# Kernel tuning notes

Measured on AMD Instinct MI355X. Metric: run time of the kernel, lower is better.

Reference implementation:

```python
import jax, jax.numpy as jnp
import numpy as np

D_MODEL = 1024
NUM_HEADS = 16
D_K = D_MODEL // NUM_HEADS
ROPE_THETA = 10000.0
BATCH = 4
SEQ = 2048


def _trunc_normal(key, shape):
    # approx of torch.nn.init.trunc_normal_ (std=1, truncated to [-2, 2])
    return jnp.clip(jax.random.truncated_normal(key, -2.0, 2.0, shape, jnp.float32), -2.0, 2.0)


def setup_inputs() -> dict:
    key = jax.random.key(0)
    kx, kq, kk, kv, ko = jax.random.split(key, 5)
    x = jax.random.normal(kx, (BATCH, SEQ, D_MODEL), jnp.float32)
    token_positions = jnp.broadcast_to(jnp.arange(SEQ, dtype=jnp.int32), (BATCH, SEQ))
    return {
        "x": x,
        "token_positions": token_positions,
        "q_proj": _trunc_normal(kq, (D_MODEL, D_MODEL)),
        "k_proj": _trunc_normal(kk, (D_MODEL, D_MODEL)),
        "v_proj": _trunc_normal(kv, (D_MODEL, D_MODEL)),
        "o_proj": _trunc_normal(ko, (D_MODEL, D_MODEL)),
    }


def _rope(t, positions):
    # t: [b, h, s, k], positions: [b, s]
    half = D_K // 2
    inv_freq = 1.0 / (ROPE_THETA ** (jnp.arange(half, dtype=jnp.float32) * 2.0 / D_K))
    ang = positions.astype(jnp.float32)[:, None, :, None] * inv_freq  # [b,1,s,half]
    cos, sin = jnp.cos(ang), jnp.sin(ang)
    t1 = t[..., 0::2]
    t2 = t[..., 1::2]
    r1 = t1 * cos - t2 * sin
    r2 = t1 * sin + t2 * cos
    return jnp.stack([r1, r2], axis=-1).reshape(t.shape)


def reference(x, token_positions, q_proj, k_proj, v_proj, o_proj):
    b, s, d = x.shape
    Wq = q_proj.reshape(NUM_HEADS, D_K, d)
    Wk = k_proj.reshape(NUM_HEADS, D_K, d)
    Wv = v_proj.reshape(NUM_HEADS, D_K, d)
    Wo = o_proj.reshape(d, NUM_HEADS, D_K).transpose(1, 0, 2)  # h d k
    Q = jnp.einsum('bsd,hkd->bhsk', x, Wq)
    K = jnp.einsum('bsd,hkd->bhsk', x, Wk)
    V = jnp.einsum('bsd,hkd->bhsk', x, Wv)
    Q = _rope(Q, token_positions)
    K = _rope(K, token_positions)
    scale = 1.0 / jnp.sqrt(jnp.asarray(D_K, jnp.float32))
    scores = jnp.einsum('bhqk,bhsk->bhqs', Q, K) * scale  # [b,h,s,s]
    causal = jnp.tril(jnp.ones((s, s), dtype=bool))
    scores = jnp.where(causal, scores, -jnp.inf)
    attn = jax.nn.softmax(scores, axis=-1)
    O = jnp.einsum('bhqs,bhsk->bhqk', attn, V)
    return jnp.einsum('bhsk,hdk->bsd', O, Wo)
```

## Files before the change

kernel.cpp:

```cpp
#include <hip/hip_runtime.h>
#include <cmath>


typedef __bf16 bf16_t;
typedef __bf16 bf16x2 __attribute__((ext_vector_type(2)));
typedef __bf16 bf16x4 __attribute__((ext_vector_type(4)));
typedef __bf16 bf16x8 __attribute__((ext_vector_type(8)));
typedef float f32x2 __attribute__((ext_vector_type(2)));
typedef float f32x4 __attribute__((ext_vector_type(4)));
typedef unsigned int u32;
typedef const __attribute__((address_space(1))) u32* gaddr_t;
typedef __attribute__((address_space(3))) u32* saddr_t;

struct RopeTab { float inv[32]; };

__device__ __forceinline__ void split4(const float* __restrict__ in,
                                       bf16_t* __restrict__ hi,
                                       bf16_t* __restrict__ lo, bool LO,
                                       int blk, int tid)
{
  const int i = blk * 256 + tid;
  const f32x4 u = *(const f32x4*)(in + (size_t)i * 4);
  bf16x4 h, l;
  #pragma unroll
  for (int j = 0; j < 4; ++j) {
    const bf16_t hb = (bf16_t)u[j];
    h[j] = hb;
    if (LO) l[j] = (bf16_t)(u[j] - (float)hb);
  }
  *(bf16x4*)(hi + (size_t)i * 4) = h;
  if (LO) *(bf16x4*)(lo + (size_t)i * 4) = l;
}

__global__ __launch_bounds__(256) void prep_k(
    const float* __restrict__ x,  const float* __restrict__ qw,
    const float* __restrict__ kw, const float* __restrict__ vw,
    const float* __restrict__ ow, RopeTab tab,
    bf16_t* __restrict__ Xh,  bf16_t* __restrict__ Xl,
    bf16_t* __restrict__ QWh, bf16_t* __restrict__ QWl,
    bf16_t* __restrict__ KWh, bf16_t* __restrict__ KWl,
    bf16_t* __restrict__ VWh, bf16_t* __restrict__ OWh,
    float* __restrict__ ropeT)
{
  const int bid = blockIdx.x, tid = threadIdx.x;
  if (bid < 8192)       split4(x,  Xh,  Xl,  true,  bid,         tid);
  else if (bid < 9216)  split4(qw, QWh, QWl, true,  bid - 8192,  tid);
  else if (bid < 10240) split4(kw, KWh, KWl, true,  bid - 9216,  tid);
  else if (bid < 11264) split4(vw, VWh, nullptr, false, bid - 10240, tid);
  else if (bid < 12288) split4(ow, OWh, nullptr, false, bid - 11264, tid);
  else {
    const int i = (bid - 12288) * 256 + tid;
    const int p = i >> 5, d2 = i & 31;
    float sn, cs;
    sincosf((float)p * tab.inv[d2], &sn, &cs);
    ropeT[(size_t)i * 2]     = cs;
    ropeT[(size_t)i * 2 + 1] = sn;
  }
}

__global__ __launch_bounds__(256, 4) void gemm_qkv(
    const bf16_t* __restrict__ Xh, const bf16_t* __restrict__ Xl,
    const bf16_t* __restrict__ QWh, const bf16_t* __restrict__ QWl,
    const bf16_t* __restrict__ KWh, const bf16_t* __restrict__ KWl,
    const bf16_t* __restrict__ VWh,
    const int* __restrict__ tokpos, const float* __restrict__ ropeT,
    bf16_t* __restrict__ Oq_h, bf16_t* __restrict__ Oq_l,
    bf16_t* __restrict__ Ok_h, bf16_t* __restrict__ Ok_l,
    bf16_t* __restrict__ Vt)
{
  __shared__ __align__(16) bf16_t sA[128 * 64];
  __shared__ __align__(16) bf16_t sB[128 * 64];

  const int tid = threadIdx.x;
  const int lane = tid & 63, wv = tid >> 6;
  const int wr = wv >> 1, wc = wv & 1;
  const int la = lane & 15, lb = lane >> 4;
  const int row0 = blockIdx.x * 128, col0 = blockIdx.y * 128;
  const int z = blockIdx.z;

  const int srow = wv * 32 + (lane >> 3);
  const int schk = lane & 7;

  f32x4 acc[4][4] = {};

  const int NT = (z == 2) ? 16 : 48;

  for (int t = 0; t < NT; ++t) {
    const int seg = t >> 4;
    const int k0 = (t & 15) << 6;
    const bf16_t* Ap = (z < 2 && seg == 2) ? Xl : Xh;
    const bf16_t* Wp = (z == 2) ? VWh
                     : (z == 1) ? ((seg == 1) ? KWl : KWh)
                                : ((seg == 1) ? QWl : QWh);
    __syncthreads();
    #pragma unroll
    for (int i = 0; i < 4; ++i) {
      const int r = srow + i * 8;
      const int cs_ = (schk ^ (r & 7)) * 8;
      __builtin_amdgcn_global_load_lds(
          (gaddr_t)(Ap + (size_t)(row0 + r) * 1024 + k0 + cs_),
          (saddr_t)(sA + wv * 2048 + i * 512), 16, 0, 0);
      __builtin_amdgcn_global_load_lds(
          (gaddr_t)(Wp + (size_t)(col0 + r) * 1024 + k0 + cs_),
          (saddr_t)(sB + wv * 2048 + i * 512), 16, 0, 0);
    }
    __syncthreads();

    #pragma unroll
    for (int ks = 0; ks < 2; ++ks) {
      bf16x8 af[4];
      #pragma unroll
      for (int m = 0; m < 4; ++m) {
        const int r = wr * 64 + m * 16 + la;
        af[m] = *(const bf16x8*)&sA[r * 64 + (((ks * 4 + lb) ^ (la & 7)) * 8)];
      }
      #pragma unroll
      for (int n = 0; n < 4; ++n) {
        const int r = wc * 64 + n * 16 + la;
        const bf16x8 bfr = *(const bf16x8*)&sB[r * 64 + (((ks * 4 + lb) ^ (la & 7)) * 8)];
        #pragma unroll
        for (int m = 0; m < 4; ++m)
          acc[m][n] = __builtin_amdgcn_mfma_f32_16x16x32_bf16(af[m], bfr, acc[m][n], 0, 0, 0);
      }
    }
  }

  #pragma unroll
  for (int n = 0; n < 4; ++n) {
    const int gn = col0 + wc * 64 + n * 16 + la;
    #pragma unroll
    for (int m = 0; m < 4; ++m) {
      const int gm0 = row0 + wr * 64 + m * 16 + lb * 4;
      if (z == 2) {
        const int b = gm0 >> 11, s0 = gm0 & 2047;
        const int h = gn >> 6, d = gn & 63;
        bf16x4 v;
        #pragma unroll
        for (int j = 0; j < 4; ++j) v[j] = (bf16_t)acc[m][n][j];
        *(bf16x4*)&Vt[(((size_t)b * 16 + h) * 64 + d) * 2048 + s0] = v;
      } else {
        const int d = gn & 63, h = gn >> 6;
        const bool odd = d & 1;
        bf16_t* Oh = z ? Ok_h : Oq_h;
        bf16_t* Ol = z ? Ok_l : Oq_l;
        #pragma unroll
        for (int j = 0; j < 4; ++j) {
          const int gm = gm0 + j;
          const float t = acc[m][n][j];
          const float other = __shfl_xor(t, 1, 64);
          const int pos = tokpos[gm];
          const f32x2 cs2 = *(const f32x2*)&ropeT[((size_t)pos << 6) + ((d >> 1) << 1)];
          const float r = odd ? (other * cs2[1] + t * cs2[0])
                              : (t * cs2[0] - other * cs2[1]);
          const bf16_t hb = (bf16_t)r;
          const int b = gm >> 11, s = gm & 2047;
          const size_t oi = (((size_t)b * 16 + h) * 2048 + s) * 64 + d;
          Oh[oi] = hb;
          Ol[oi] = (bf16_t)(r - (float)hb);
        }
      }
    }
  }
}

__global__ __launch_bounds__(256, 4) void gemm_o(
    const bf16_t* __restrict__ Ag, const bf16_t* __restrict__ Wg,
    float* __restrict__ Of)
{
  __shared__ __align__(16) bf16_t sA[128 * 64];
  __shared__ __align__(16) bf16_t sB[128 * 64];

  const int tid = threadIdx.x;
  const int lane = tid & 63, wv = tid >> 6;
  const int wr = wv >> 1, wc = wv & 1;
  const int la = lane & 15, lb = lane >> 4;
  const int row0 = blockIdx.x * 128, col0 = blockIdx.y * 128;

  const int srow = wv * 32 + (lane >> 3);
  const int schk = lane & 7;

  f32x4 acc[4][4] = {};

  for (int t = 0; t < 16; ++t) {
    const int k0 = t << 6;
    __syncthreads();
    #pragma unroll
    for (int i = 0; i < 4; ++i) {
      const int r = srow + i * 8;
      const int cs_ = (schk ^ (r & 7)) * 8;
      __builtin_amdgcn_global_load_lds(
          (gaddr_t)(Ag + (size_t)(row0 + r) * 1024 + k0 + cs_),
          (saddr_t)(sA + wv * 2048 + i * 512), 16, 0, 0);
      __builtin_amdgcn_global_load_lds(
          (gaddr_t)(Wg + (size_t)(col0 + r) * 1024 + k0 + cs_),
          (saddr_t)(sB + wv * 2048 + i * 512), 16, 0, 0);
    }
    __syncthreads();
    #pragma unroll
    for (int ks = 0; ks < 2; ++ks) {
      bf16x8 af[4];
      #pragma unroll
      for (int m = 0; m < 4; ++m) {
        const int r = wr * 64 + m * 16 + la;
        af[m] = *(const bf16x8*)&sA[r * 64 + (((ks * 4 + lb) ^ (la & 7)) * 8)];
      }
      #pragma unroll
      for (int n = 0; n < 4; ++n) {
        const int r = wc * 64 + n * 16 + la;
        const bf16x8 bfr = *(const bf16x8*)&sB[r * 64 + (((ks * 4 + lb) ^ (la & 7)) * 8)];
        #pragma unroll
        for (int m = 0; m < 4; ++m)
          acc[m][n] = __builtin_amdgcn_mfma_f32_16x16x32_bf16(af[m], bfr, acc[m][n], 0, 0, 0);
      }
    }
  }

  #pragma unroll
  for (int n = 0; n < 4; ++n) {
    const int gn = col0 + wc * 64 + n * 16 + la;
    #pragma unroll
    for (int m = 0; m < 4; ++m) {
      const int gm0 = row0 + wr * 64 + m * 16 + lb * 4;
      #pragma unroll
      for (int j = 0; j < 4; ++j)
        Of[(size_t)(gm0 + j) * 1024 + gn] = acc[m][n][j];
    }
  }
}

__device__ __forceinline__ int SW(int e) { return e ^ (((e >> 6) & 7) << 3); }

__global__ __launch_bounds__(512, 4) void attn_kernel(
    const bf16_t* __restrict__ Qhi, const bf16_t* __restrict__ Qlo,
    const bf16_t* __restrict__ Khi, const bf16_t* __restrict__ Klo,
    const bf16_t* __restrict__ Vt, bf16_t* __restrict__ O)
{
  __shared__ __align__(16) bf16_t sKV[2][3 * 4096];
  __shared__ __align__(16) bf16_t sP[8 * 1024];

  const int linear = (int)blockIdx.x;
  const int xcd = linear & 7;
  const int pos = linear >> 3;
  const int bh  = xcd * 8 + (pos >> 3);
  const int p   = pos & 7;
  const int b = bh >> 4, h = bh & 15;

  const size_t base = (size_t)bh * 2048 * 64;
  const bf16_t* Qh_ = Qhi + base;
  const bf16_t* Ql_ = Qlo + base;
  const bf16_t* Kh_ = Khi + base;
  const bf16_t* Kl_ = Klo + base;
  const bf16_t* Vt_ = Vt + base;

  const int tid = threadIdx.x, wv = tid >> 6, lane = tid & 63;
  const int la = lane & 15, lb = lane >> 4;

  const int sr   = wv * 8 + (lane >> 3);
  const int scsw = (lane & 7) ^ (sr & 7);
  const int ssrc = sr * 64 + scsw * 8;
  const int se0  = wv * 512;
  const int psw  = (la & 7) << 3;

  auto STAGE = [&](int kvb, int buf) {
    const int kv0 = kvb * 64;
    bf16_t* dst = &sKV[buf][0];
    __builtin_amdgcn_global_load_lds((gaddr_t)(Kh_ + (size_t)kv0 * 64 + ssrc),
                                     (saddr_t)(dst + se0), 16, 0, 0);
    __builtin_amdgcn_global_load_lds((gaddr_t)(Kl_ + (size_t)kv0 * 64 + ssrc),
                                     (saddr_t)(dst + 4096 + se0), 16, 0, 0);
    __builtin_amdgcn_global_load_lds((gaddr_t)(Vt_ + (size_t)sr * 2048 + kv0 + scsw * 8),
                                     (saddr_t)(dst + 8192 + se0), 16, 0, 0);
  };

  for (int half = 0; half < 2; ++half) {
    const int qb = half ? p : 15 - p;
    const int q = qb * 128 + wv * 16 + la;
    bf16x8 qh[2], ql[2];
    #pragma unroll
    for (int kf = 0; kf < 2; ++kf) {
      qh[kf] = *(const bf16x8*)&Qh_[(size_t)q * 64 + kf * 32 + lb * 8];
      ql[kf] = *(const bf16x8*)&Ql_[(size_t)q * 64 + kf * 32 + lb * 8];
    }

    f32x4 oacc[4] = {};
    float m = -1e30f, l = 0.f;
    const int nt = 2 * qb + 2;

    STAGE(0, 0);
    __syncthreads();

    for (int kvb = 0; kvb < nt; ++kvb) {
      const int kv0 = kvb * 64;
      if (kvb + 1 < nt) STAGE(kvb + 1, (kvb + 1) & 1);

      const bf16_t* sKh = &sKV[kvb & 1][0];
      const bf16_t* sKl = sKh + 4096;
      const bf16_t* sVt = sKh + 8192;

      f32x4 sacc[4] = {};
      __builtin_amdgcn_s_setprio(1);
      #pragma unroll
      for (int nf = 0; nf < 4; ++nf) {
        #pragma unroll
        for (int kf = 0; kf < 2; ++kf) {
          const int rr = SW((nf * 16 + la) * 64 + kf * 32 + lb * 8);
          const bf16x8 kh = *(const bf16x8*)&sKh[rr];
          const bf16x8 kl = *(const bf16x8*)&sKl[rr];
          sacc[nf] = __builtin_amdgcn_mfma_f32_16x16x32_bf16(kh, qh[kf], sacc[nf], 0, 0, 0);
          sacc[nf] = __builtin_amdgcn_mfma_f32_16x16x32_bf16(kl, qh[kf], sacc[nf], 0, 0, 0);
          sacc[nf] = __builtin_amdgcn_mfma_f32_16x16x32_bf16(kh, ql[kf], sacc[nf], 0, 0, 0);
        }
      }
      __builtin_amdgcn_s_setprio(0);

      if (kvb >= 2 * qb) {
        #pragma unroll
        for (int nf = 0; nf < 4; ++nf)
          #pragma unroll
          for (int j = 0; j < 4; ++j) {
            const int kvi = kv0 + nf * 16 + lb * 4 + j;
            sacc[nf][j] = (kvi <= q) ? sacc[nf][j] * 0.125f : -1e30f;
          }
      } else {
        #pragma unroll
        for (int nf = 0; nf < 4; ++nf)
          #pragma unroll
          for (int j = 0; j < 4; ++j) sacc[nf][j] *= 0.125f;
      }

      float red = sacc[0][0];
      #pragma unroll
      for (int nf = 0; nf < 4; ++nf)
        #pragma unroll
        for (int j = 0; j < 4; ++j) red = fmaxf(red, sacc[nf][j]);
      red = fmaxf(red, __shfl_xor(red, 16, 64));
      red = fmaxf(red, __shfl_xor(red, 32, 64));

      const float mn = fmaxf(m, red);
      if (!__all(mn - m <= 8.0f)) {
        const float sf = __expf(m - mn);
        m = mn;
        l *= sf;
        #pragma unroll
        for (int nf = 0; nf < 4; ++nf)
          #pragma unroll
          for (int j = 0; j < 4; ++j) oacc[nf][j] *= sf;
      }

      float rs = 0.f;
      #pragma unroll
      for (int nf = 0; nf < 4; ++nf)
        #pragma unroll
        for (int j = 0; j < 4; ++j) {
          const float pj = __expf(sacc[nf][j] - m);
          sacc[nf][j] = pj;
          rs += pj;
        }
      rs += __shfl_xor(rs, 16, 64);
      rs += __shfl_xor(rs, 32, 64);
      l += rs;

      #pragma unroll
      for (int nf = 0; nf < 4; ++nf) {
        bf16x4 pv;
        #pragma unroll
        for (int j = 0; j < 4; ++j) pv[j] = (bf16_t)sacc[nf][j];
        *(bf16x4*)&sP[wv * 1024 + la * 64 + ((nf * 16 + lb * 4) ^ psw)] = pv;
      }

      __builtin_amdgcn_s_setprio(1);
      #pragma unroll
      for (int ks = 0; ks < 2; ++ks) {
        const bf16x8 pa = *(const bf16x8*)&sP[wv * 1024 + la * 64 + ((ks * 32 + lb * 8) ^ psw)];
        #pragma unroll
        for (int nf = 0; nf < 4; ++nf) {
          const bf16x8 vb2 = *(const bf16x8*)&sVt[SW((nf * 16 + la) * 64 + ks * 32 + lb * 8)];
          oacc[nf] = __builtin_amdgcn_mfma_f32_16x16x32_bf16(vb2, pa, oacc[nf], 0, 0, 0);
        }
      }
      __builtin_amdgcn_s_setprio(0);

      __syncthreads();
    }

    const float inv_l = 1.0f / l;
    #pragma unroll
    for (int nf = 0; nf < 4; ++nf) {
      bf16x4 ov;
      #pragma unroll
      for (int j = 0; j < 4; ++j) ov[j] = (bf16_t)(oacc[nf][j] * inv_l);
      const int d0 = nf * 16 + lb * 4;
      *(bf16x4*)&O[(((size_t)b * 2048 + q) * 16 + h) * 64 + d0] = ov;
    }
  }
}

extern "C" void kernel_launch(void* const* d_in, const int* in_sizes, int n_in,
                              void* d_out, int out_size, void* d_ws, size_t ws_size,
                              hipStream_t stream)
{
  const float* x      = (const float*)d_in[0];
  const int*   tokpos = (const int*)d_in[1];
  const float* qw     = (const float*)d_in[2];
  const float* kw     = (const float*)d_in[3];
  const float* vw     = (const float*)d_in[4];
  const float* ow     = (const float*)d_in[5];
  float* out = (float*)d_out;

  const size_t E  = (size_t)4 * 16 * 2048 * 64;
  const size_t W1 = (size_t)1024 * 1024;
  bf16_t* base = (bf16_t*)d_ws;
  bf16_t* Qhi = base;
  bf16_t* Qlo = base + E;
  bf16_t* Khi = base + 2 * E;
  bf16_t* Klo = base + 3 * E;
  bf16_t* Vt  = base + 4 * E;
  bf16_t* Xh  = base + 5 * E;
  bf16_t* Xl  = base + 6 * E;
  bf16_t* QWh = base + 7 * E;
  bf16_t* QWl = QWh + W1;
  bf16_t* KWh = QWh + 2 * W1;
  bf16_t* KWl = QWh + 3 * W1;
  bf16_t* VWh = QWh + 4 * W1;
  bf16_t* OWh = QWh + 5 * W1;
  float*  ropeT = (float*)(QWh + 6 * W1);
  bf16_t* O = Xh;

  RopeTab tab;
  for (int i = 0; i < 32; ++i)
    tab.inv[i] = (float)pow(10000.0, -(double)i / 32.0);

  prep_k<<<12544, 256, 0, stream>>>(x, qw, kw, vw, ow, tab,
                                    Xh, Xl, QWh, QWl, KWh, KWl, VWh, OWh, ropeT);

  gemm_qkv<<<dim3(64, 8, 3), 256, 0, stream>>>(
      Xh, Xl, QWh, QWl, KWh, KWl, VWh, tokpos, ropeT,
      Qhi, Qlo, Khi, Klo, Vt);
  attn_kernel<<<512, 512, 0, stream>>>(Qhi, Qlo, Khi, Klo, Vt, O);
  gemm_o<<<dim3(64, 8), 256, 0, stream>>>(O, OWh, out);
}
```

Measured before the change: 241.7 us.

## Add 256x256 double-buffered Q/K projection GEMM with async LDS loads

The Q and K projections move into a new kernel with 256x256 output tiles, 512 threads, double-buffered shared memory filled by direct global-to-LDS loads, XOR-swizzled layout, tile-index remapping and setprio around the MFMA loop. The V projection stays on the old kernel, launched separately with a z offset. The larger tiles are meant to raise arithmetic intensity and overlap loads with compute. The cost is one block per CU (128 blocks per z slice on a 256-CU part), a second kernel launch, and an epilogue that writes the RoPE'd outputs as scattered scalar stores.

New measurement: 282.0 us. 1.17x slower.

```diff
diff --git a/kernel.cpp b/kernel.cpp
--- a/kernel.cpp
+++ b/kernel.cpp
@@ -58,6 +58,121 @@
   }
 }
 
+__global__ __launch_bounds__(512, 1) void gemm_qk256(
+    const bf16_t* __restrict__ Xh, const bf16_t* __restrict__ Xl,
+    const bf16_t* __restrict__ QWh, const bf16_t* __restrict__ QWl,
+    const bf16_t* __restrict__ KWh, const bf16_t* __restrict__ KWl,
+    const int* __restrict__ tokpos, const float* __restrict__ ropeT,
+    bf16_t* __restrict__ Oq_h, bf16_t* __restrict__ Oq_l,
+    bf16_t* __restrict__ Ok_h, bf16_t* __restrict__ Ok_l)
+{
+  __shared__ __align__(16) bf16_t sA[2][256 * 64];
+  __shared__ __align__(16) bf16_t sB[2][256 * 64];
+
+  const int tid = threadIdx.x;
+  const int lane = tid & 63, wv = tid >> 6;
+  const int wr = wv >> 2, wc = wv & 3;
+  const int la = lane & 15, lb = lane >> 4;
+
+  const int lin  = (int)blockIdx.y * 32 + (int)blockIdx.x;
+  const int lin2 = (lin & 7) * 16 + (lin >> 3);
+  const int bx = lin2 & 31, by = lin2 >> 5;
+  const int row0 = bx * 256, col0 = by * 256;
+  const int z = blockIdx.z;
+
+  const bf16_t* Wh = z ? KWh : QWh;
+  const bf16_t* Wl = z ? KWl : QWl;
+
+  const int sr8  = tid >> 3;
+  const int scsw = (tid & 7) ^ (sr8 & 7);
+
+  f32x4 acc[8][4] = {};
+
+  auto STAGE = [&](int t, int buf) {
+    const int seg = t >> 4;
+    const int k0 = (t & 15) << 6;
+    const bf16_t* Ap = (seg == 2) ? Xl : Xh;
+    const bf16_t* Wp = (seg == 1) ? Wl : Wh;
+    #pragma unroll
+    for (int j = 0; j < 4; ++j) {
+      const int r = j * 64 + sr8;
+      __builtin_amdgcn_global_load_lds(
+          (gaddr_t)(Ap + (size_t)(row0 + r) * 1024 + k0 + scsw * 8),
+          (saddr_t)(&sA[buf][0] + j * 4096 + tid * 8), 16, 0, 0);
+    }
+    #pragma unroll
+    for (int j = 0; j < 4; ++j) {
+      const int r = j * 64 + sr8;
+      __builtin_amdgcn_global_load_lds(
+          (gaddr_t)(Wp + (size_t)(col0 + r) * 1024 + k0 + scsw * 8),
+          (saddr_t)(&sB[buf][0] + j * 4096 + tid * 8), 16, 0, 0);
+    }
+  };
+
+  const int NT = 48;
+  STAGE(0, 0);
+  for (int t = 0; t < NT; ++t) {
+    if (t + 1 < NT) {
+      STAGE(t + 1, (t + 1) & 1);
+      asm volatile("s_waitcnt vmcnt(8)" ::: "memory");
+    } else {
+      asm volatile("s_waitcnt vmcnt(0)" ::: "memory");
+    }
+    __builtin_amdgcn_s_barrier();
+
+    const bf16_t* cA = &sA[t & 1][0];
+    const bf16_t* cB = &sB[t & 1][0];
+    #pragma unroll
+    for (int ks = 0; ks < 2; ++ks) {
+      bf16x8 bfr[4];
+      #pragma unroll
+      for (int nf = 0; nf < 4; ++nf) {
+        const int r = wc * 64 + nf * 16 + la;
+        bfr[nf] = *(const bf16x8*)&cB[r * 64 + (((ks * 4 + lb) ^ (la & 7)) * 8)];
+      }
+      __builtin_amdgcn_s_setprio(1);
+      #pragma unroll
+      for (int mf = 0; mf < 8; ++mf) {
+        const int r = wr * 128 + mf * 16 + la;
+        const bf16x8 a = *(const bf16x8*)&cA[r * 64 + (((ks * 4 + lb) ^ (la & 7)) * 8)];
+        #pragma unroll
+        for (int nf = 0; nf < 4; ++nf)
+          acc[mf][nf] = __builtin_amdgcn_mfma_f32_16x16x32_bf16(a, bfr[nf], acc[mf][nf], 0, 0, 0);
+      }
+      __builtin_amdgcn_s_setprio(0);
+    }
+    __builtin_amdgcn_s_barrier();
+  }
+
+  bf16_t* Oh = z ? Ok_h : Oq_h;
+  bf16_t* Ol = z ? Ok_l : Oq_l;
+  #pragma unroll
+  for (int n = 0; n < 4; ++n) {
+    const int gn = col0 + wc * 64 + n * 16 + la;
+    const int d = gn & 63, h = gn >> 6;
+    const bool odd = d & 1;
+    #pragma unroll
+    for (int m = 0; m < 8; ++m) {
+      const int gm0 = row0 + wr * 128 + m * 16 + lb * 4;
+      #pragma unroll
+      for (int j = 0; j < 4; ++j) {
+        const int gm = gm0 + j;
+        const float t = acc[m][n][j];
+        const float other = __shfl_xor(t, 1, 64);
+        const int pos = tokpos[gm];
+        const f32x2 cs2 = *(const f32x2*)&ropeT[((size_t)pos << 6) + ((d >> 1) << 1)];
+        const float r = odd ? (other * cs2[1] + t * cs2[0])
+                            : (t * cs2[0] - other * cs2[1]);
+        const bf16_t hb = (bf16_t)r;
+        const int b = gm >> 11, s = gm & 2047;
+        const size_t oi = (((size_t)b * 16 + h) * 2048 + s) * 64 + d;
+        Oh[oi] = hb;
+        Ol[oi] = (bf16_t)(r - (float)hb);
+      }
+    }
+  }
+}
+
 __global__ __launch_bounds__(256, 4) void gemm_qkv(
     const bf16_t* __restrict__ Xh, const bf16_t* __restrict__ Xl,
     const bf16_t* __restrict__ QWh, const bf16_t* __restrict__ QWl,
@@ -66,7 +181,7 @@
     const int* __restrict__ tokpos, const float* __restrict__ ropeT,
     bf16_t* __restrict__ Oq_h, bf16_t* __restrict__ Oq_l,
     bf16_t* __restrict__ Ok_h, bf16_t* __restrict__ Ok_l,
-    bf16_t* __restrict__ Vt)
+    bf16_t* __restrict__ Vt, int zbase)
 {
   __shared__ __align__(16) bf16_t sA[128 * 64];
   __shared__ __align__(16) bf16_t sB[128 * 64];
@@ -76,7 +191,7 @@
   const int wr = wv >> 1, wc = wv & 1;
   const int la = lane & 15, lb = lane >> 4;
   const int row0 = blockIdx.x * 128, col0 = blockIdx.y * 128;
-  const int z = blockIdx.z;
+  const int z = blockIdx.z + zbase;
 
   const int srow = wv * 32 + (lane >> 3);
   const int schk = lane & 7;
@@ -433,9 +548,11 @@
   prep_k<<<12544, 256, 0, stream>>>(x, qw, kw, vw, ow, tab,
                                     Xh, Xl, QWh, QWl, KWh, KWl, VWh, OWh, ropeT);
 
-  gemm_qkv<<<dim3(64, 8, 3), 256, 0, stream>>>(
+  gemm_qk256<<<dim3(32, 4, 2), 512, 0, stream>>>(
+      Xh, Xl, QWh, QWl, KWh, KWl, tokpos, ropeT, Qhi, Qlo, Khi, Klo);
+  gemm_qkv<<<dim3(64, 8, 1), 256, 0, stream>>>(
       Xh, Xl, QWh, QWl, KWh, KWl, VWh, tokpos, ropeT,
-      Qhi, Qlo, Khi, Klo, Vt);
+      Qhi, Qlo, Khi, Klo, Vt, 2);
   attn_kernel<<<512, 512, 0, stream>>>(Qhi, Qlo, Khi, Klo, Vt, O);
   gemm_o<<<dim3(64, 8), 256, 0, stream>>>(O, OWh, out);
 }
```

## Fuse Q and K projections into one block sharing the X tile

Applied to the files above, without the earlier changes.

The QKV GEMM now runs with 512-thread blocks. In the z=0 slice, two groups of four waves compute Q and K for the same 128x128 tile and share one staged X tile in LDS, which halves X reloads for the Q/K projections. The V projection uses 8 waves on a 128x128 tile with 4x2 accumulators per wave. The grid shrinks from 3 to 2 z-slices. This costs more LDS per block (48KB) and leaves the two z-slices with unequal work (48 k-steps vs 16), which may hurt load balance.

Result: slower. 249.7 us (+3.3%).

```diff
diff --git a/kernel.cpp b/kernel.cpp
--- a/kernel.cpp
+++ b/kernel.cpp
@@ -58,7 +58,7 @@
   }
 }
 
-__global__ __launch_bounds__(256, 4) void gemm_qkv(
+__global__ __launch_bounds__(512, 4) void gemm_qkv2(
     const bf16_t* __restrict__ Xh, const bf16_t* __restrict__ Xl,
     const bf16_t* __restrict__ QWh, const bf16_t* __restrict__ QWl,
     const bf16_t* __restrict__ KWh, const bf16_t* __restrict__ KWl,
@@ -69,80 +69,75 @@
     bf16_t* __restrict__ Vt)
 {
   __shared__ __align__(16) bf16_t sA[128 * 64];
-  __shared__ __align__(16) bf16_t sB[128 * 64];
+  __shared__ __align__(16) bf16_t sW0[128 * 64];
+  __shared__ __align__(16) bf16_t sW1[128 * 64];
 
   const int tid = threadIdx.x;
   const int lane = tid & 63, wv = tid >> 6;
-  const int wr = wv >> 1, wc = wv & 1;
   const int la = lane & 15, lb = lane >> 4;
   const int row0 = blockIdx.x * 128, col0 = blockIdx.y * 128;
-  const int z = blockIdx.z;
-
-  const int srow = wv * 32 + (lane >> 3);
-  const int schk = lane & 7;
-
-  f32x4 acc[4][4] = {};
-
-  const int NT = (z == 2) ? 16 : 48;
-
-  for (int t = 0; t < NT; ++t) {
-    const int seg = t >> 4;
-    const int k0 = (t & 15) << 6;
-    const bf16_t* Ap = (z < 2 && seg == 2) ? Xl : Xh;
-    const bf16_t* Wp = (z == 2) ? VWh
-                     : (z == 1) ? ((seg == 1) ? KWl : KWh)
-                                : ((seg == 1) ? QWl : QWh);
-    __syncthreads();
-    #pragma unroll
-    for (int i = 0; i < 4; ++i) {
-      const int r = srow + i * 8;
-      const int cs_ = (schk ^ (r & 7)) * 8;
-      __builtin_amdgcn_global_load_lds(
-          (gaddr_t)(Ap + (size_t)(row0 + r) * 1024 + k0 + cs_),
-          (saddr_t)(sA + wv * 2048 + i * 512), 16, 0, 0);
-      __builtin_amdgcn_global_load_lds(
-          (gaddr_t)(Wp + (size_t)(col0 + r) * 1024 + k0 + cs_),
-          (saddr_t)(sB + wv * 2048 + i * 512), 16, 0, 0);
-    }
-    __syncthreads();
-
-    #pragma unroll
-    for (int ks = 0; ks < 2; ++ks) {
-      bf16x8 af[4];
+
+  const int c0 = tid, c1 = 512 + tid;
+  const int r0 = c0 >> 3, r1 = c1 >> 3;
+  const int cs0 = ((c0 & 7) ^ (r0 & 7)) * 8;
+  const int cs1 = ((c1 & 7) ^ (r1 & 7)) * 8;
+  const int db0 = wv * 512;
+  const int db1 = 4096 + wv * 512;
+
+  if (blockIdx.z == 0) {
+    const int grp = wv >> 2, wq = wv & 3;
+    const int wr = wq >> 1, wc = wq & 1;
+    f32x4 acc[4][4] = {};
+
+    for (int t = 0; t < 48; ++t) {
+      const int seg = t >> 4;
+      const int k0 = (t & 15) << 6;
+      const bf16_t* Ap = (seg == 2) ? Xl : Xh;
+      const bf16_t* Qp = (seg == 1) ? QWl : QWh;
+      const bf16_t* Kp = (seg == 1) ? KWl : KWh;
+      __syncthreads();
+      __builtin_amdgcn_global_load_lds(
+          (gaddr_t)(Ap + (size_t)(row0 + r0) * 1024 + k0 + cs0), (saddr_t)(sA + db0), 16, 0, 0);
+      __builtin_amdgcn_global_load_lds(
+          (gaddr_t)(Ap + (size_t)(row0 + r1) * 1024 + k0 + cs1), (saddr_t)(sA + db1), 16, 0, 0);
+      __builtin_amdgcn_global_load_lds(
+          (gaddr_t)(Qp + (size_t)(col0 + r0) * 1024 + k0 + cs0), (saddr_t)(sW0 + db0), 16, 0, 0);
+      __builtin_amdgcn_global_load_lds(
+          (gaddr_t)(Qp + (size_t)(col0 + r1) * 1024 + k0 + cs1), (saddr_t)(sW0 + db1), 16, 0, 0);
+      __builtin_amdgcn_global_load_lds(
+          (gaddr_t)(Kp + (size_t)(col0 + r0) * 1024 + k0 + cs0), (saddr_t)(sW1 + db0), 16, 0, 0);
+      __builtin_amdgcn_global_load_lds(
+          (gaddr_t)(Kp + (size_t)(col0 + r1) * 1024 + k0 + cs1), (saddr_t)(sW1 + db1), 16, 0, 0);
+      __syncthreads();
+
+      const bf16_t* sW = grp ? sW1 : sW0;
+      #pragma unroll
+      for (int ks = 0; ks < 2; ++ks) {
+        const int kcol = ((ks * 4 + lb) ^ (la & 7)) * 8;
+        bf16x8 af[4];
+        #pragma unroll
+        for (int m = 0; m < 4; ++m)
+          af[m] = *(const bf16x8*)&sA[(wr * 64 + m * 16 + la) * 64 + kcol];
+        #pragma unroll
+        for (int n = 0; n < 4; ++n) {
+          const bf16x8 bfr = *(const bf16x8*)&sW[(wc * 64 + n * 16 + la) * 64 + kcol];
+          #pragma unroll
+          for (int m = 0; m < 4; ++m)
+            acc[m][n] = __builtin_amdgcn_mfma_f32_16x16x32_bf16(af[m], bfr, acc[m][n], 0, 0, 0);
+        }
+      }
+    }
+
+    bf16_t* Oh = grp ? Ok_h : Oq_h;
+    bf16_t* Ol = grp ? Ok_l : Oq_l;
+    #pragma unroll
+    for (int n = 0; n < 4; ++n) {
+      const int gn = col0 + wc * 64 + n * 16 + la;
+      const int d = gn & 63, h = gn >> 6;
+      const bool odd = d & 1;
       #pragma unroll
       for (int m = 0; m < 4; ++m) {
-        const int r = wr * 64 + m * 16 + la;
-        af[m] = *(const bf16x8*)&sA[r * 64 + (((ks * 4 + lb) ^ (la & 7)) * 8)];
-      }
-      #pragma unroll
-      for (int n = 0; n < 4; ++n) {
-        const int r = wc * 64 + n * 16 + la;
-        const bf16x8 bfr = *(const bf16x8*)&sB[r * 64 + (((ks * 4 + lb) ^ (la & 7)) * 8)];
-        #pragma unroll
-        for (int m = 0; m < 4; ++m)
-          acc[m][n] = __builtin_amdgcn_mfma_f32_16x16x32_bf16(af[m], bfr, acc[m][n], 0, 0, 0);
-      }
-    }
-  }
-
-  #pragma unroll
-  for (int n = 0; n < 4; ++n) {
-    const int gn = col0 + wc * 64 + n * 16 + la;
-    #pragma unroll
-    for (int m = 0; m < 4; ++m) {
-      const int gm0 = row0 + wr * 64 + m * 16 + lb * 4;
-      if (z == 2) {
-        const int b = gm0 >> 11, s0 = gm0 & 2047;
-        const int h = gn >> 6, d = gn & 63;
-        bf16x4 v;
-        #pragma unroll
-        for (int j = 0; j < 4; ++j) v[j] = (bf16_t)acc[m][n][j];
-        *(bf16x4*)&Vt[(((size_t)b * 16 + h) * 64 + d) * 2048 + s0] = v;
-      } else {
-        const int d = gn & 63, h = gn >> 6;
-        const bool odd = d & 1;
-        bf16_t* Oh = z ? Ok_h : Oq_h;
-        bf16_t* Ol = z ? Ok_l : Oq_l;
+        const int gm0 = row0 + wr * 64 + m * 16 + lb * 4;
         #pragma unroll
         for (int j = 0; j < 4; ++j) {
           const int gm = gm0 + j;
@@ -158,6 +153,54 @@
           Oh[oi] = hb;
           Ol[oi] = (bf16_t)(r - (float)hb);
         }
+      }
+    }
+  } else {
+    const int wr = wv >> 2, wc = wv & 3;
+    f32x4 acc[4][2] = {};
+
+    for (int t = 0; t < 16; ++t) {
+      const int k0 = t << 6;
+      __syncthreads();
+      __builtin_amdgcn_global_load_lds(
+          (gaddr_t)(Xh + (size_t)(row0 + r0) * 1024 + k0 + cs0), (saddr_t)(sA + db0), 16, 0, 0);
+      __builtin_amdgcn_global_load_lds(
+          (gaddr_t)(Xh + (size_t)(row0 + r1) * 1024 + k0 + cs1), (saddr_t)(sA + db1), 16, 0, 0);
+      __builtin_amdgcn_global_load_lds(
+          (gaddr_t)(VWh + (size_t)(col0 + r0) * 1024 + k0 + cs0), (saddr_t)(sW0 + db0), 16, 0, 0);
+      __builtin_amdgcn_global_load_lds(
+          (gaddr_t)(VWh + (size_t)(col0 + r1) * 1024 + k0 + cs1), (saddr_t)(sW0 + db1), 16, 0, 0);
+      __syncthreads();
+
+      #pragma unroll
+      for (int ks = 0; ks < 2; ++ks) {
+        const int kcol = ((ks * 4 + lb) ^ (la & 7)) * 8;
+        bf16x8 af[4];
+        #pragma unroll
+        for (int m = 0; m < 4; ++m)
+          af[m] = *(const bf16x8*)&sA[(wr * 64 + m * 16 + la) * 64 + kcol];
+        #pragma unroll
+        for (int n = 0; n < 2; ++n) {
+          const bf16x8 bfr = *(const bf16x8*)&sW0[(wc * 32 + n * 16 + la) * 64 + kcol];
+          #pragma unroll
+          for (int m = 0; m < 4; ++m)
+            acc[m][n] = __builtin_amdgcn_mfma_f32_16x16x32_bf16(af[m], bfr, acc[m][n], 0, 0, 0);
+        }
+      }
+    }
+
+    #pragma unroll
+    for (int n = 0; n < 2; ++n) {
+      const int gn = col0 + wc * 32 + n * 16 + la;
+      const int h = gn >> 6, d = gn & 63;
+      #pragma unroll
+      for (int m = 0; m < 4; ++m) {
+        const int gm0 = row0 + wr * 64 + m * 16 + lb * 4;
+        const int b = gm0 >> 11, s0 = gm0 & 2047;
+        bf16x4 v;
+        #pragma unroll
+        for (int j = 0; j < 4; ++j) v[j] = (bf16_t)acc[m][n][j];
+        *(bf16x4*)&Vt[(((size_t)b * 16 + h) * 64 + d) * 2048 + s0] = v;
       }
     }
   }
@@ -433,7 +476,7 @@
   prep_k<<<12544, 256, 0, stream>>>(x, qw, kw, vw, ow, tab,
                                     Xh, Xl, QWh, QWl, KWh, KWl, VWh, OWh, ropeT);
 
-  gemm_qkv<<<dim3(64, 8, 3), 256, 0, stream>>>(
+  gemm_qkv2<<<dim3(64, 8, 2), 512, 0, stream>>>(
       Xh, Xl, QWh, QWl, KWh, KWl, VWh, tokpos, ropeT,
       Qhi, Qlo, Khi, Klo, Vt);
   attn_kernel<<<512, 512, 0, stream>>>(Qhi, Qlo, Khi, Klo, Vt, O);
```
